# Kernel optimization log

Hardware: AMD Instinct MI355X
Metric: run time of the kernel (lower is better)

The kernel has to match this reference:

```python
import jax, jax.numpy as jnp
import numpy as np

H = 12  # max_heads

def setup_inputs() -> dict:
    key = jax.random.key(0)
    ks = jax.random.split(key, 5)
    B, N, E = 8, 1024, 768
    return {
        "x": jax.random.normal(ks[0], (B, N, E), dtype=jnp.float32),
        "w_qkv": jax.random.normal(ks[1], (3 * E, E), dtype=jnp.float32) * 0.02,
        "b_qkv": jax.random.normal(ks[2], (3 * E,), dtype=jnp.float32) * 0.02,
        "w_proj": jax.random.normal(ks[3], (E, E), dtype=jnp.float32) * 0.02,
        "b_proj": jax.random.normal(ks[4], (E,), dtype=jnp.float32) * 0.02,
        "active_heads": 8,
    }

def reference(x, w_qkv, b_qkv, w_proj, b_proj, active_heads):
    B, N, E = x.shape
    D = E // H
    scale = D ** -0.5
    # qkv projection: [B,N,3E] -> [3,B,H,N,D]
    qkv = (x @ w_qkv.T + b_qkv).reshape(B, N, 3, H, D)
    qkv = jnp.transpose(qkv, (2, 0, 3, 1, 4))
    q, k, v = qkv[0], qkv[1], qkv[2]
    # head mask from active_heads (static int)
    head_mask = (jnp.arange(H) < active_heads).astype(x.dtype)
    m = head_mask[None, :, None, None]
    q = q * m
    k = k * m
    v = v * m
    attn = jax.nn.softmax(jnp.einsum("bhqd,bhkd->bhqk", q, k) * scale, axis=-1)
    out = jnp.einsum("bhqk,bhkd->bhqd", attn, v)
    out = jnp.transpose(out, (0, 2, 1, 3)).reshape(B, N, E)
    channel_mask = jnp.repeat(head_mask, D)  # [E]
    out = out * channel_mask[None, None, :]
    return out @ w_proj.T + b_proj
```

## Files before the change

kernel.cpp:

```cpp
#include <hip/hip_runtime.h>
#include <hip/hip_fp16.h>

#define NH 12
#define BSZ 8
#define NSEQ 1024
#define EDIM 768
#define DH 64

typedef _Float16 f16;
typedef f16 half8 __attribute__((ext_vector_type(8)));
typedef f16 half4 __attribute__((ext_vector_type(4)));
typedef float f32x4 __attribute__((ext_vector_type(4)));
typedef unsigned int u32;
typedef u32 u32x2 __attribute__((ext_vector_type(2)));

static __device__ __forceinline__ void gload16(const void* g, void* l) {
    __builtin_amdgcn_global_load_lds((const __attribute__((address_space(1))) u32*)g,
                                     (__attribute__((address_space(3))) u32*)l, 16, 0, 0);
}
static __device__ __forceinline__ u32 pkrtz(float a, float b) {
    auto h = __builtin_amdgcn_cvt_pkrtz(a, b);
    return __builtin_bit_cast(u32, h);
}
#define MFMA16(a, b, c) __builtin_amdgcn_mfma_f32_16x16x32_f16((a), (b), (c), 0, 0, 0)

__global__ void cvt_all_kernel(const float* __restrict__ x, const float* __restrict__ wq,
                               const float* __restrict__ wp, f16* __restrict__ dst) {
    const int NX = BSZ * NSEQ * EDIM;
    const int NWQ = 3 * EDIM * EDIM;
    int i = (blockIdx.x * blockDim.x + threadIdx.x) * 4;
    const float* s;
    int j;
    if (i < NX) { s = x; j = i; }
    else if (i < NX + NWQ) { s = wq; j = i - NX; }
    else { s = wp; j = i - NX - NWQ; }
    float4 v = *(const float4*)(s + j);
    half4 o = { (f16)v.x, (f16)v.y, (f16)v.z, (f16)v.w };
    *(half4*)(dst + i) = o;
}

template<int MODE>
__global__ __launch_bounds__(512) void gemm_kernel(
    const f16* __restrict__ A, const f16* __restrict__ Wt, const float* __restrict__ bias,
    f16* __restrict__ qbuf, f16* __restrict__ kbuf, f16* __restrict__ vbuf,
    float* __restrict__ outp, const int* __restrict__ activep, int Kd, int NCd)
{
    __shared__ __align__(16) f16 Ah[2][2][4][64][8];
    __shared__ __align__(16) f16 Bh[2][4][4][64][8];

    constexpr int K = EDIM;
    constexpr int NKT = K / 32;
    constexpr int NB = (MODE == 0) ? 9 : 3;

    const int lin = blockIdx.x;
    const int xcd = lin & 7, pos = lin >> 3;
    const int bx = pos % NB;
    const int my = xcd + (pos / NB) * 8;
    const int c0 = bx * 256;
    const int m0 = my * 128;
    const int ah = *activep;
    if (MODE == 0) {
        if (((c0 % EDIM) >> 6) >= ah) return;
    }
    const int tid = threadIdx.x;
    const int lane = tid & 63;
    const int wid  = tid >> 6;
    const int wr = wid >> 2;
    const int wc = wid & 3;
    const int r16 = lane & 15, rg = lane >> 4;

    f32x4 acc[4][4];
#pragma unroll
    for (int i = 0; i < 4; ++i)
#pragma unroll
        for (int j = 0; j < 4; ++j)
            acc[i][j] = f32x4{0.f, 0.f, 0.f, 0.f};

    const int awrh = wid >> 2, afm = wid & 3;
    const int ib0 = 2 * wid, ib1 = 2 * wid + 1;
    const f16* gAs  = A  + (size_t)(m0 + awrh * 64 + afm * 16 + r16) * K + rg * 8;
    const f16* gBs0 = Wt + (size_t)(c0 + (ib0 >> 2) * 64 + (ib0 & 3) * 16 + r16) * K + rg * 8;
    const f16* gBs1 = Wt + (size_t)(c0 + (ib1 >> 2) * 64 + (ib1 & 3) * 16 + r16) * K + rg * 8;

    auto stage = [&](int buf, int kt) {
        gload16(gAs  + kt * 32, &Ah[buf][awrh][afm][0][0]);
        gload16(gBs0 + kt * 32, &Bh[buf][ib0 >> 2][ib0 & 3][0][0]);
        gload16(gBs1 + kt * 32, &Bh[buf][ib1 >> 2][ib1 & 3][0][0]);
    };

    stage(0, 0);
    stage(1, 1);
    asm volatile("s_waitcnt vmcnt(3)" ::: "memory");
    __builtin_amdgcn_s_barrier();
    __builtin_amdgcn_sched_barrier(0);

#pragma unroll 1
    for (int kt = 0; kt < NKT; ++kt) {
        const int cur = kt & 1;
        half8 af[4], bf[4];
#pragma unroll
        for (int f = 0; f < 4; ++f) {
            af[f] = *(const half8*)&Ah[cur][wr][f][lane][0];
            bf[f] = *(const half8*)&Bh[cur][wc][f][lane][0];
        }
        asm volatile("s_waitcnt lgkmcnt(0)" ::: "memory");
        __builtin_amdgcn_sched_barrier(0);
        __builtin_amdgcn_s_barrier();
        __builtin_amdgcn_sched_barrier(0);
        if (kt + 2 < NKT) stage(cur, kt + 2);
        __builtin_amdgcn_sched_barrier(0);
        __builtin_amdgcn_s_setprio(1);
#pragma unroll
        for (int fm = 0; fm < 4; ++fm)
#pragma unroll
            for (int fn = 0; fn < 4; ++fn)
                acc[fm][fn] = MFMA16(af[fm], bf[fn], acc[fm][fn]);
        __builtin_amdgcn_s_setprio(0);
        if (kt + 1 < NKT) {
            if (kt + 2 < NKT) asm volatile("s_waitcnt vmcnt(3)" ::: "memory");
            else              asm volatile("s_waitcnt vmcnt(0)" ::: "memory");
            __builtin_amdgcn_s_barrier();
            __builtin_amdgcn_sched_barrier(0);
        }
    }

#pragma unroll
    for (int fn = 0; fn < 4; ++fn) {
        const int c = c0 + wc * 64 + fn * 16 + r16;
        const float bv = bias[c];
        const bool colActive = (MODE == 1) || (((c % EDIM) >> 6) < ah);
#pragma unroll
        for (int fm = 0; fm < 4; ++fm) {
            const int mbase = m0 + wr * 64 + fm * 16 + rg * 4;
#pragma unroll
            for (int r = 0; r < 4; ++r) {
                const float val = acc[fm][fn][r] + bv;
                const int m = mbase + r;
                if (MODE == 1) {
                    outp[(size_t)m * EDIM + c] = val;
                } else if (colActive) {
                    const int s  = c / EDIM;
                    const int cc = c % EDIM;
                    const int hh = cc >> 6, d = cc & 63;
                    const int bb = m >> 10, n = m & 1023;
                    f16* dst = (s == 0) ? qbuf : ((s == 1) ? kbuf : vbuf);
                    dst[(((size_t)bb * NH + hh) * NSEQ + n) * DH + d] = (f16)val;
                }
            }
        }
    }
}

__global__ __launch_bounds__(256) void vtrans_kernel(const f16* __restrict__ vbuf,
                                                     f16* __restrict__ vtb,
                                                     const int* __restrict__ activep) {
    const int b = blockIdx.z, h = blockIdx.y;
    if (h >= *activep) return;
    const int n0 = blockIdx.x * 64;
    __shared__ __align__(16) f16 T[64][72];
    const f16* src = vbuf + (((size_t)b * NH + h) * NSEQ + n0) * DH;
    f16* dst = vtb + ((size_t)b * NH + h) * DH * NSEQ;
    const int t = threadIdx.x;
    const int rn = t >> 2, rc = t & 3;
    *(half8*)&T[rn][rc * 16]     = *(const half8*)&src[(size_t)rn * DH + rc * 16];
    *(half8*)&T[rn][rc * 16 + 8] = *(const half8*)&src[(size_t)rn * DH + rc * 16 + 8];
    __syncthreads();
    const int d = t >> 2, nc = (t & 3) * 16;
    half8 o0, o1;
#pragma unroll
    for (int j = 0; j < 8; ++j) {
        o0[j] = T[nc + j][d];
        o1[j] = T[nc + 8 + j][d];
    }
    *(half8*)&dst[(size_t)d * NSEQ + n0 + nc]     = o0;
    *(half8*)&dst[(size_t)d * NSEQ + n0 + nc + 8] = o1;
}

__global__ __launch_bounds__(512) void attn_kernel(
    const f16* __restrict__ qbuf, const f16* __restrict__ kbuf, const f16* __restrict__ vtb,
    f16* __restrict__ ctx, const int* __restrict__ activep)
{
    __shared__ __align__(16) f16 Kh[2][64][64];
    __shared__ __align__(16) f16 Vh[2][64][64];
    __shared__ __align__(16) f16 Ph[8][16][64];

    const int b = blockIdx.z, h = blockIdx.y;
    const int q0 = blockIdx.x * 128;
    const int tid = threadIdx.x, lane = tid & 63, wid = tid >> 6;

    if (h >= *activep) {
        const int r = tid >> 2, cp = tid & 3;
        half8 z = { (f16)0,(f16)0,(f16)0,(f16)0,(f16)0,(f16)0,(f16)0,(f16)0 };
        size_t base = ((size_t)b * NSEQ + q0 + r) * EDIM + h * DH + cp * 16;
        *(half8*)&ctx[base]     = z;
        *(half8*)&ctx[base + 8] = z;
        return;
    }

    const size_t hb = (((size_t)b * NH + h) * NSEQ) * DH;
    const f16* Q  = qbuf + hb;
    const char* Kp = (const char*)(kbuf + hb);
    const char* Vp = (const char*)(vtb + hb);

    const int ql = lane & 15;
    const int g  = lane >> 4;
    const int q7 = ql & 7;

    half8 qb0, qb1;
    {
        const f16 qsc = (f16)0.18033688f;
        const f16* qp = Q + (size_t)(q0 + wid * 16 + ql) * DH + g * 8;
        qb0 = *(const half8*)qp        * qsc;
        qb1 = *(const half8*)(qp + 32) * qsc;
    }

    const int srow8 = lane >> 3;
    const int schk  = (lane & 7) ^ srow8;
    const int qh4   = wid & 3;

    auto stage = [&](int buf, int kt) {
        if (wid < 4) {
            const char* kb = Kp + (size_t)kt * 8192;
#pragma unroll
            for (int i = 0; i < 2; ++i) {
                const int r = qh4 * 16 + i * 8 + srow8;
                gload16(kb + (size_t)r * 128 + schk * 16, &Kh[buf][qh4 * 16 + i * 8][0]);
            }
        } else {
#pragma unroll
            for (int i = 0; i < 2; ++i) {
                const int r = qh4 * 16 + i * 8 + srow8;
                gload16(Vp + (size_t)r * (NSEQ * 2) + (size_t)kt * 128 + schk * 16,
                        &Vh[buf][qh4 * 16 + i * 8][0]);
            }
        }
    };

    f32x4 oacc[4];
#pragma unroll
    for (int i = 0; i < 4; ++i) oacc[i] = f32x4{0.f, 0.f, 0.f, 0.f};
    float mr = -INFINITY, lr = 0.f;

    char* prow = (char*)&Ph[wid][ql][0];

    stage(0, 0);
    const int NT = NSEQ / 64;
    for (int kt = 0; kt < NT; ++kt) {
        const int cur = kt & 1;
        __syncthreads();
        if (kt + 1 < NT) stage(cur ^ 1, kt + 1);

        f32x4 st[4];
        __builtin_amdgcn_s_setprio(1);
#pragma unroll
        for (int s = 0; s < 4; ++s) {
            f32x4 t = f32x4{0.f, 0.f, 0.f, 0.f};
            t = MFMA16(*(const half8*)((const char*)&Kh[cur][16 * s + ql][0] + ((g ^ q7) << 4)),       qb0, t);
            t = MFMA16(*(const half8*)((const char*)&Kh[cur][16 * s + ql][0] + (((4 | g) ^ q7) << 4)), qb1, t);
            st[s] = t;
        }
        __builtin_amdgcn_s_setprio(0);

        float a0 = fmaxf(fmaxf(st[0][0], st[0][1]), st[0][2]);
        float a1 = fmaxf(fmaxf(st[0][3], st[1][0]), st[1][1]);
        float a2 = fmaxf(fmaxf(st[1][2], st[1][3]), st[2][0]);
        float a3 = fmaxf(fmaxf(st[2][1], st[2][2]), st[2][3]);
        float a4 = fmaxf(fmaxf(st[3][0], st[3][1]), st[3][2]);
        float pmax = fmaxf(fmaxf(fmaxf(a0, a1), fmaxf(a2, a3)), fmaxf(a4, st[3][3]));
        pmax = fmaxf(pmax, __shfl_xor(pmax, 16));
        pmax = fmaxf(pmax, __shfl_xor(pmax, 32));

        const float mnew = fmaxf(mr, pmax);
        const float sc = exp2f(mr - mnew);
        float psum = 0.f;
#pragma unroll
        for (int s = 0; s < 4; ++s)
#pragma unroll
            for (int r = 0; r < 4; ++r) {
                float p = exp2f(st[s][r] - mnew);
                st[s][r] = p;
                psum += p;
            }
        psum += __shfl_xor(psum, 16);
        psum += __shfl_xor(psum, 32);
        lr = lr * sc + psum;
        mr = mnew;

#pragma unroll
        for (int r = 0; r < 4; ++r) {
            const float scr = __shfl(sc, (g << 2) | r);
            oacc[0][r] *= scr; oacc[1][r] *= scr; oacc[2][r] *= scr; oacc[3][r] *= scr;
        }

#pragma unroll
        for (int s = 0; s < 4; ++s) {
            u32x2 w = { pkrtz(st[s][0], st[s][1]), pkrtz(st[s][2], st[s][3]) };
            *(u32x2*)(prow + ((32 * s + 8 * g) ^ (q7 << 4))) = w;
        }
        const half8 pa0 = *(const half8*)(prow + ((16 * g) ^ (q7 << 4)));
        const half8 pa1 = *(const half8*)(prow + ((64 + 16 * g) ^ (q7 << 4)));

        __builtin_amdgcn_s_setprio(1);
#pragma unroll
        for (int db = 0; db < 4; ++db) {
            oacc[db] = MFMA16(pa0, *(const half8*)((const char*)&Vh[cur][16 * db + ql][0] + ((g ^ q7) << 4)),       oacc[db]);
            oacc[db] = MFMA16(pa1, *(const half8*)((const char*)&Vh[cur][16 * db + ql][0] + (((4 | g) ^ q7) << 4)), oacc[db]);
        }
        __builtin_amdgcn_s_setprio(0);
    }

#pragma unroll
    for (int r = 0; r < 4; ++r) {
        const float li = 1.0f / __shfl(lr, (g << 2) | r);
        const int n = q0 + wid * 16 + (g << 2) + r;
#pragma unroll
        for (int db = 0; db < 4; ++db)
            ctx[((size_t)b * NSEQ + n) * EDIM + h * DH + db * 16 + ql] = (f16)(oacc[db][r] * li);
    }
}

extern "C" void kernel_launch(void* const* d_in, const int* in_sizes, int n_in,
                              void* d_out, int out_size, void* d_ws, size_t ws_size,
                              hipStream_t stream) {
    const float* x      = (const float*)d_in[0];
    const float* w_qkv  = (const float*)d_in[1];
    const float* b_qkv  = (const float*)d_in[2];
    const float* w_proj = (const float*)d_in[3];
    const float* b_proj = (const float*)d_in[4];
    const int*   active = (const int*)d_in[5];
    float* out = (float*)d_out;

    char* ws = (char*)d_ws;
    const size_t n_x  = (size_t)BSZ * NSEQ * EDIM;
    const size_t n_wq = (size_t)3 * EDIM * EDIM;
    const size_t n_wp = (size_t)EDIM * EDIM;
    const size_t n_hd = (size_t)BSZ * NH * NSEQ * DH;

    f16* xh   = (f16*)ws;
    f16* wqh  = xh + n_x;
    f16* wph  = wqh + n_wq;
    f16* qh   = wph + n_wp;
    f16* kh   = qh + n_hd;
    f16* vh   = kh + n_hd;
    f16* ctxh = vh + n_hd;
    f16* vtb  = xh;

    const size_t n_cvt = n_x + n_wq + n_wp;
    cvt_all_kernel<<<(int)(n_cvt / 4 / 256), 256, 0, stream>>>(x, w_qkv, w_proj, xh);

    gemm_kernel<0><<<dim3(64 * 9), 512, 0, stream>>>(
        xh, wqh, b_qkv, qh, kh, vh, nullptr, active, EDIM, 3 * EDIM);

    vtrans_kernel<<<dim3(NSEQ / 64, NH, BSZ), 256, 0, stream>>>(vh, vtb, active);

    attn_kernel<<<dim3(NSEQ / 128, NH, BSZ), 512, 0, stream>>>(qh, kh, vtb, ctxh, active);

    gemm_kernel<1><<<dim3(64 * 3), 512, 0, stream>>>(
        ctxh, wph, b_proj, nullptr, nullptr, nullptr, out, active, EDIM, EDIM);
}
```

Measured before the change: 129.0 us.

## Fuse V transpose into QKV GEMM, skip inactive-head K range and zero stores

The QKV GEMM epilogue now writes V directly in transposed [d][n] layout, which removes the separate transpose kernel and its extra global round trip. The output projection GEMM truncates its K loop to the active heads' channels (2*active_heads tiles of 32), so the masked zero columns of ctx are never read. Because of that, attention no longer zero-fills ctx for inactive heads. The softmax row sum is now computed with an MFMA against a ones vector instead of VALU adds and shuffles. The transposed V stores are strided, which risks poorly coalesced writes, and correctness relies on the K-truncation lining up with the zero-fill that was removed.

Result: slower. 134.4 us (+4.1%).

```diff
diff --git a/kernel.cpp b/kernel.cpp
--- a/kernel.cpp
+++ b/kernel.cpp
@@ -42,7 +42,7 @@
 template<int MODE>
 __global__ __launch_bounds__(512) void gemm_kernel(
     const f16* __restrict__ A, const f16* __restrict__ Wt, const float* __restrict__ bias,
-    f16* __restrict__ qbuf, f16* __restrict__ kbuf, f16* __restrict__ vbuf,
+    f16* __restrict__ qbuf, f16* __restrict__ kbuf, f16* __restrict__ vtbuf,
     float* __restrict__ outp, const int* __restrict__ activep, int Kd, int NCd)
 {
     __shared__ __align__(16) f16 Ah[2][2][4][64][8];
@@ -62,6 +62,7 @@
     if (MODE == 0) {
         if (((c0 % EDIM) >> 6) >= ah) return;
     }
+    const int nkt = (MODE == 1) ? (2 * ah) : NKT;
     const int tid = threadIdx.x;
     const int lane = tid & 63;
     const int wid  = tid >> 6;
@@ -95,7 +96,7 @@
     __builtin_amdgcn_sched_barrier(0);
 
 #pragma unroll 1
-    for (int kt = 0; kt < NKT; ++kt) {
+    for (int kt = 0; kt < nkt; ++kt) {
         const int cur = kt & 1;
         half8 af[4], bf[4];
 #pragma unroll
@@ -107,7 +108,7 @@
         __builtin_amdgcn_sched_barrier(0);
         __builtin_amdgcn_s_barrier();
         __builtin_amdgcn_sched_barrier(0);
-        if (kt + 2 < NKT) stage(cur, kt + 2);
+        if (kt + 2 < nkt) stage(cur, kt + 2);
         __builtin_amdgcn_sched_barrier(0);
         __builtin_amdgcn_s_setprio(1);
 #pragma unroll
@@ -116,8 +117,8 @@
             for (int fn = 0; fn < 4; ++fn)
                 acc[fm][fn] = MFMA16(af[fm], bf[fn], acc[fm][fn]);
         __builtin_amdgcn_s_setprio(0);
-        if (kt + 1 < NKT) {
-            if (kt + 2 < NKT) asm volatile("s_waitcnt vmcnt(3)" ::: "memory");
+        if (kt + 1 < nkt) {
+            if (kt + 2 < nkt) asm volatile("s_waitcnt vmcnt(3)" ::: "memory");
             else              asm volatile("s_waitcnt vmcnt(0)" ::: "memory");
             __builtin_amdgcn_s_barrier();
             __builtin_amdgcn_sched_barrier(0);
@@ -143,37 +144,16 @@
                     const int cc = c % EDIM;
                     const int hh = cc >> 6, d = cc & 63;
                     const int bb = m >> 10, n = m & 1023;
-                    f16* dst = (s == 0) ? qbuf : ((s == 1) ? kbuf : vbuf);
-                    dst[(((size_t)bb * NH + hh) * NSEQ + n) * DH + d] = (f16)val;
+                    if (s == 2) {
+                        vtbuf[(((size_t)bb * NH + hh) * DH + d) * NSEQ + n] = (f16)val;
+                    } else {
+                        f16* dst = (s == 0) ? qbuf : kbuf;
+                        dst[(((size_t)bb * NH + hh) * NSEQ + n) * DH + d] = (f16)val;
+                    }
                 }
             }
         }
     }
-}
-
-__global__ __launch_bounds__(256) void vtrans_kernel(const f16* __restrict__ vbuf,
-                                                     f16* __restrict__ vtb,
-                                                     const int* __restrict__ activep) {
-    const int b = blockIdx.z, h = blockIdx.y;
-    if (h >= *activep) return;
-    const int n0 = blockIdx.x * 64;
-    __shared__ __align__(16) f16 T[64][72];
-    const f16* src = vbuf + (((size_t)b * NH + h) * NSEQ + n0) * DH;
-    f16* dst = vtb + ((size_t)b * NH + h) * DH * NSEQ;
-    const int t = threadIdx.x;
-    const int rn = t >> 2, rc = t & 3;
-    *(half8*)&T[rn][rc * 16]     = *(const half8*)&src[(size_t)rn * DH + rc * 16];
-    *(half8*)&T[rn][rc * 16 + 8] = *(const half8*)&src[(size_t)rn * DH + rc * 16 + 8];
-    __syncthreads();
-    const int d = t >> 2, nc = (t & 3) * 16;
-    half8 o0, o1;
-#pragma unroll
-    for (int j = 0; j < 8; ++j) {
-        o0[j] = T[nc + j][d];
-        o1[j] = T[nc + 8 + j][d];
-    }
-    *(half8*)&dst[(size_t)d * NSEQ + n0 + nc]     = o0;
-    *(half8*)&dst[(size_t)d * NSEQ + n0 + nc + 8] = o1;
 }
 
 __global__ __launch_bounds__(512) void attn_kernel(
@@ -188,14 +168,7 @@
     const int q0 = blockIdx.x * 128;
     const int tid = threadIdx.x, lane = tid & 63, wid = tid >> 6;
 
-    if (h >= *activep) {
-        const int r = tid >> 2, cp = tid & 3;
-        half8 z = { (f16)0,(f16)0,(f16)0,(f16)0,(f16)0,(f16)0,(f16)0,(f16)0 };
-        size_t base = ((size_t)b * NSEQ + q0 + r) * EDIM + h * DH + cp * 16;
-        *(half8*)&ctx[base]     = z;
-        *(half8*)&ctx[base + 8] = z;
-        return;
-    }
+    if (h >= *activep) return;
 
     const size_t hb = (((size_t)b * NH + h) * NSEQ) * DH;
     const f16* Q  = qbuf + hb;
@@ -213,6 +186,7 @@
         qb0 = *(const half8*)qp        * qsc;
         qb1 = *(const half8*)(qp + 32) * qsc;
     }
+    const half8 ones = { (f16)1, (f16)1, (f16)1, (f16)1, (f16)1, (f16)1, (f16)1, (f16)1 };
 
     const int srow8 = lane >> 3;
     const int schk  = (lane & 7) ^ srow8;
@@ -239,7 +213,8 @@
     f32x4 oacc[4];
 #pragma unroll
     for (int i = 0; i < 4; ++i) oacc[i] = f32x4{0.f, 0.f, 0.f, 0.f};
-    float mr = -INFINITY, lr = 0.f;
+    f32x4 lacc = f32x4{0.f, 0.f, 0.f, 0.f};
+    float mr = -INFINITY;
 
     char* prow = (char*)&Ph[wid][ql][0];
 
@@ -272,24 +247,18 @@
 
         const float mnew = fmaxf(mr, pmax);
         const float sc = exp2f(mr - mnew);
-        float psum = 0.f;
 #pragma unroll
         for (int s = 0; s < 4; ++s)
 #pragma unroll
-            for (int r = 0; r < 4; ++r) {
-                float p = exp2f(st[s][r] - mnew);
-                st[s][r] = p;
-                psum += p;
-            }
-        psum += __shfl_xor(psum, 16);
-        psum += __shfl_xor(psum, 32);
-        lr = lr * sc + psum;
+            for (int r = 0; r < 4; ++r)
+                st[s][r] = exp2f(st[s][r] - mnew);
         mr = mnew;
 
 #pragma unroll
         for (int r = 0; r < 4; ++r) {
             const float scr = __shfl(sc, (g << 2) | r);
             oacc[0][r] *= scr; oacc[1][r] *= scr; oacc[2][r] *= scr; oacc[3][r] *= scr;
+            lacc[r] *= scr;
         }
 
 #pragma unroll
@@ -301,6 +270,8 @@
         const half8 pa1 = *(const half8*)(prow + ((64 + 16 * g) ^ (q7 << 4)));
 
         __builtin_amdgcn_s_setprio(1);
+        lacc = MFMA16(pa0, ones, lacc);
+        lacc = MFMA16(pa1, ones, lacc);
 #pragma unroll
         for (int db = 0; db < 4; ++db) {
             oacc[db] = MFMA16(pa0, *(const half8*)((const char*)&Vh[cur][16 * db + ql][0] + ((g ^ q7) << 4)),       oacc[db]);
@@ -311,7 +282,7 @@
 
 #pragma unroll
     for (int r = 0; r < 4; ++r) {
-        const float li = 1.0f / __shfl(lr, (g << 2) | r);
+        const float li = 1.0f / lacc[r];
         const int n = q0 + wid * 16 + (g << 2) + r;
 #pragma unroll
         for (int db = 0; db < 4; ++db)
@@ -341,19 +312,16 @@
     f16* wph  = wqh + n_wq;
     f16* qh   = wph + n_wp;
     f16* kh   = qh + n_hd;
-    f16* vh   = kh + n_hd;
-    f16* ctxh = vh + n_hd;
-    f16* vtb  = xh;
+    f16* vth  = kh + n_hd;
+    f16* ctxh = vth + n_hd;
 
     const size_t n_cvt = n_x + n_wq + n_wp;
     cvt_all_kernel<<<(int)(n_cvt / 4 / 256), 256, 0, stream>>>(x, w_qkv, w_proj, xh);
 
     gemm_kernel<0><<<dim3(64 * 9), 512, 0, stream>>>(
-        xh, wqh, b_qkv, qh, kh, vh, nullptr, active, EDIM, 3 * EDIM);
-
-    vtrans_kernel<<<dim3(NSEQ / 64, NH, BSZ), 256, 0, stream>>>(vh, vtb, active);
-
-    attn_kernel<<<dim3(NSEQ / 128, NH, BSZ), 512, 0, stream>>>(qh, kh, vtb, ctxh, active);
+        xh, wqh, b_qkv, qh, kh, vth, nullptr, active, EDIM, 3 * EDIM);
+
+    attn_kernel<<<dim3(NSEQ / 128, NH, BSZ), 512, 0, stream>>>(qh, kh, vth, ctxh, active);
 
     gemm_kernel<1><<<dim3(64 * 3), 512, 0, stream>>>(
         ctxh, wph, b_proj, nullptr, nullptr, nullptr, out, active, EDIM, EDIM);
```

## Truncate projection K-loop to active heads and compute softmax rowsum via MFMA

Applied to the files above, without the earlier changes.

The output projection GEMM now loops only over the K tiles that belong to active heads (2*active_heads tiles of 32), skipping the masked channels. Because of that, the attention kernel no longer writes zeros into ctx for inactive heads and simply returns. Separately, the softmax denominator is accumulated by an extra MFMA of the fp16 P tile against a ones vector. This replaces the per-lane exp sums and cross-lane shuffles and keeps the denominator consistent with the rounded numerator. The cost is two more MFMAs per key tile, and ctx for inactive heads is now left uninitialised, so any reader that ignores active_heads would see garbage.

After: 118.6 us. 8.1% less time.

```diff
diff --git a/kernel.cpp b/kernel.cpp
--- a/kernel.cpp
+++ b/kernel.cpp
@@ -62,6 +62,7 @@
     if (MODE == 0) {
         if (((c0 % EDIM) >> 6) >= ah) return;
     }
+    const int nkt = (MODE == 1) ? (2 * ah) : NKT;
     const int tid = threadIdx.x;
     const int lane = tid & 63;
     const int wid  = tid >> 6;
@@ -95,7 +96,7 @@
     __builtin_amdgcn_sched_barrier(0);
 
 #pragma unroll 1
-    for (int kt = 0; kt < NKT; ++kt) {
+    for (int kt = 0; kt < nkt; ++kt) {
         const int cur = kt & 1;
         half8 af[4], bf[4];
 #pragma unroll
@@ -107,7 +108,7 @@
         __builtin_amdgcn_sched_barrier(0);
         __builtin_amdgcn_s_barrier();
         __builtin_amdgcn_sched_barrier(0);
-        if (kt + 2 < NKT) stage(cur, kt + 2);
+        if (kt + 2 < nkt) stage(cur, kt + 2);
         __builtin_amdgcn_sched_barrier(0);
         __builtin_amdgcn_s_setprio(1);
 #pragma unroll
@@ -116,8 +117,8 @@
             for (int fn = 0; fn < 4; ++fn)
                 acc[fm][fn] = MFMA16(af[fm], bf[fn], acc[fm][fn]);
         __builtin_amdgcn_s_setprio(0);
-        if (kt + 1 < NKT) {
-            if (kt + 2 < NKT) asm volatile("s_waitcnt vmcnt(3)" ::: "memory");
+        if (kt + 1 < nkt) {
+            if (kt + 2 < nkt) asm volatile("s_waitcnt vmcnt(3)" ::: "memory");
             else              asm volatile("s_waitcnt vmcnt(0)" ::: "memory");
             __builtin_amdgcn_s_barrier();
             __builtin_amdgcn_sched_barrier(0);
@@ -188,14 +189,7 @@
     const int q0 = blockIdx.x * 128;
     const int tid = threadIdx.x, lane = tid & 63, wid = tid >> 6;
 
-    if (h >= *activep) {
-        const int r = tid >> 2, cp = tid & 3;
-        half8 z = { (f16)0,(f16)0,(f16)0,(f16)0,(f16)0,(f16)0,(f16)0,(f16)0 };
-        size_t base = ((size_t)b * NSEQ + q0 + r) * EDIM + h * DH + cp * 16;
-        *(half8*)&ctx[base]     = z;
-        *(half8*)&ctx[base + 8] = z;
-        return;
-    }
+    if (h >= *activep) return;
 
     const size_t hb = (((size_t)b * NH + h) * NSEQ) * DH;
     const f16* Q  = qbuf + hb;
@@ -213,6 +207,7 @@
         qb0 = *(const half8*)qp        * qsc;
         qb1 = *(const half8*)(qp + 32) * qsc;
     }
+    const half8 ones = { (f16)1, (f16)1, (f16)1, (f16)1, (f16)1, (f16)1, (f16)1, (f16)1 };
 
     const int srow8 = lane >> 3;
     const int schk  = (lane & 7) ^ srow8;
@@ -239,7 +234,8 @@
     f32x4 oacc[4];
 #pragma unroll
     for (int i = 0; i < 4; ++i) oacc[i] = f32x4{0.f, 0.f, 0.f, 0.f};
-    float mr = -INFINITY, lr = 0.f;
+    f32x4 lacc = f32x4{0.f, 0.f, 0.f, 0.f};
+    float mr = -INFINITY;
 
     char* prow = (char*)&Ph[wid][ql][0];
 
@@ -272,24 +268,18 @@
 
         const float mnew = fmaxf(mr, pmax);
         const float sc = exp2f(mr - mnew);
-        float psum = 0.f;
 #pragma unroll
         for (int s = 0; s < 4; ++s)
 #pragma unroll
-            for (int r = 0; r < 4; ++r) {
-                float p = exp2f(st[s][r] - mnew);
-                st[s][r] = p;
-                psum += p;
-            }
-        psum += __shfl_xor(psum, 16);
-        psum += __shfl_xor(psum, 32);
-        lr = lr * sc + psum;
+            for (int r = 0; r < 4; ++r)
+                st[s][r] = exp2f(st[s][r] - mnew);
         mr = mnew;
 
 #pragma unroll
         for (int r = 0; r < 4; ++r) {
             const float scr = __shfl(sc, (g << 2) | r);
             oacc[0][r] *= scr; oacc[1][r] *= scr; oacc[2][r] *= scr; oacc[3][r] *= scr;
+            lacc[r] *= scr;
         }
 
 #pragma unroll
@@ -301,6 +291,8 @@
         const half8 pa1 = *(const half8*)(prow + ((64 + 16 * g) ^ (q7 << 4)));
 
         __builtin_amdgcn_s_setprio(1);
+        lacc = MFMA16(pa0, ones, lacc);
+        lacc = MFMA16(pa1, ones, lacc);
 #pragma unroll
         for (int db = 0; db < 4; ++db) {
             oacc[db] = MFMA16(pa0, *(const half8*)((const char*)&Vh[cur][16 * db + ql][0] + ((g ^ q7) << 4)),       oacc[db]);
@@ -311,7 +303,7 @@
 
 #pragma unroll
     for (int r = 0; r < 4; ++r) {
-        const float li = 1.0f / __shfl(lr, (g << 2) | r);
+        const float li = 1.0f / lacc[r];
         const int n = q0 + wid * 16 + (g << 2) + r;
 #pragma unroll
         for (int db = 0; db < 4; ++db)
```
